# Kernel optimization log

Hardware: AMD Instinct MI355X
Metric: run time of the kernel (lower is better)

Reference implementation:

```python
import jax, jax.numpy as jnp
from jax import lax
import numpy as np

B, T, C_IN, H, W = 2, 4, 128, 64, 64
D_MODEL, N_Q, N_POINTS, PATCH, N_LAYERS = 256, 300, 8, 3, 6


def _sine_pos(Hh, Ww, d, temperature=10000.0):
    # mask is all-False, so cumsum of ones -> arange(1..H)/H * 2pi
    two_pi = 2.0 * np.pi
    yn = (jnp.arange(1, Hh + 1, dtype=jnp.float32) / (Hh + 1e-6)) * two_pi
    xn = (jnp.arange(1, Ww + 1, dtype=jnp.float32) / (Ww + 1e-6)) * two_pi
    q = d // 4
    i = jnp.arange(q, dtype=jnp.float32)
    dim_t = temperature ** (2.0 * jnp.floor(i / 2.0) / q)
    py = yn[:, None] / dim_t
    px = xn[:, None] / dim_t
    py = jnp.stack([jnp.sin(py), jnp.cos(py)], axis=-1).reshape(Hh, 2 * q)
    px = jnp.stack([jnp.sin(px), jnp.cos(px)], axis=-1).reshape(Ww, 2 * q)
    pos = jnp.concatenate([
        jnp.broadcast_to(py[:, None, :], (Hh, Ww, 2 * q)),
        jnp.broadcast_to(px[None, :, :], (Hh, Ww, 2 * q)),
    ], axis=-1)
    return jnp.transpose(pos, (2, 0, 1))  # [d,H,W]


def _sample_scale(fmap, ref, ps):
    # fmap [B,C,h,w]; ref [B,nQ,nP,2] in [0,1]. Bilinear grid_sample,
    # padding_mode='border', align_corners=True -> direct gather (no replication).
    Bc, C, h, w = fmap.shape
    half = (ps - 1) / 2.0
    off = jnp.linspace(-half, half, ps, dtype=jnp.float32)
    oy, ox = jnp.meshgrid(off, off, indexing='ij')  # [ps,ps]
    gx = ref[..., 0, None, None] * 2.0 - 1.0 + ox * (2.0 / w)  # [B,nQ,nP,ps,ps]
    gy = ref[..., 1, None, None] * 2.0 - 1.0 + oy * (2.0 / h)
    x = jnp.clip((gx + 1.0) * 0.5 * (w - 1), 0.0, w - 1.0)
    y = jnp.clip((gy + 1.0) * 0.5 * (h - 1), 0.0, h - 1.0)
    x0 = jnp.floor(x); y0 = jnp.floor(y)
    wx = x - x0; wy = y - y0
    x0i = x0.astype(jnp.int32); y0i = y0.astype(jnp.int32)
    x1i = jnp.minimum(x0i + 1, w - 1); y1i = jnp.minimum(y0i + 1, h - 1)

    def per_b(fb, y0b, x0b, y1b, x1b, wxb, wyb):
        v00 = fb[:, y0b, x0b]  # [C,nQ,nP,ps,ps]
        v01 = fb[:, y0b, x1b]
        v10 = fb[:, y1b, x0b]
        v11 = fb[:, y1b, x1b]
        return (v00 * (1 - wxb) * (1 - wyb) + v01 * wxb * (1 - wyb)
                + v10 * (1 - wxb) * wyb + v11 * wxb * wyb)

    out = jax.vmap(per_b)(fmap, y0i, x0i, y1i, x1i, wx, wy)  # [B,C,nQ,nP,ps,ps]
    return jnp.transpose(out, (0, 2, 3, 4, 5, 1))  # [B,nQ,nP,ps,ps,C]


def reference(feat, pred_boxes_init, w_tf, b_tf, w_in, b_in, w_lat, b_lat, w_sm, b_sm,
              q_embed, q_pos, Wq, bq, Wo, bo, Wp1, bp1, Wp2, bp2,
              w_r1, b_r1, w_r2, b_r2, w_b1, b_b1, w_b2, b_b2, w_cls, b_cls):
    Bb, Tt, Cin, Hh, Ww = feat.shape
    d = w_in.shape[0]
    nP = w_r2.shape[0] // 2
    ps = int(round((Wp1.shape[-1] // d) ** 0.5))
    # temporal fuse: Conv3d kernel (3,1,1), padding (1,0,0)
    x = lax.conv_general_dilated(jnp.transpose(feat, (0, 2, 1, 3, 4)), w_tf,
                                 (1, 1, 1), [(1, 1), (0, 0), (0, 0)],
                                 dimension_numbers=('NCDHW', 'OIDHW', 'NCDHW'))
    x = x + b_tf[None, :, None, None, None]
    x = x.mean(axis=2)  # [B,Cin,H,W]
    x = jnp.einsum('bchw,dc->bdhw', x, w_in) + b_in[None, :, None, None]
    x = x + _sine_pos(Hh, Ww, d)[None]
    # FPN over scales {1,2,4}: avg_pool -> 1x1 lateral -> 3x3 smooth
    feats = []
    for i, s in enumerate((1, 2, 4)):
        xi = x if s == 1 else x.reshape(Bb, d, Hh // s, s, Ww // s, s).mean(axis=(3, 5))
        xi = jnp.einsum('bchw,oc->bohw', xi, w_lat[i]) + b_lat[i][None, :, None, None]
        xi = lax.conv_general_dilated(xi, w_sm[i], (1, 1), [(1, 1), (1, 1)],
                                      dimension_numbers=('NCHW', 'OIHW', 'NCHW'))
        xi = xi + b_sm[i][None, :, None, None]
        feats.append(xi)
    nQ = q_embed.shape[0]
    queries = jnp.broadcast_to((q_embed + q_pos)[None], (Bb, nQ, d))
    boxes = pred_boxes_init
    inv_sqrt_d = 1.0 / float(np.sqrt(d))
    for l in range(Wq.shape[0]):
        h1 = jax.nn.relu(jnp.einsum('bqd,od->bqo', queries, w_r1) + b_r1)
        ro = jnp.tanh(jnp.einsum('bqd,od->bqo', h1, w_r2) + b_r2)
        ro = ro.reshape(Bb, nQ, nP, 2) * 0.5
        ref = jnp.clip(boxes[:, :, None, :2] + ro, 0.0, 1.0)
        sampled = jnp.concatenate([_sample_scale(f, ref, ps) for f in feats], axis=2)
        sampled = sampled[:, :, :nP]  # truncate multi-scale concat back to nP
        flat = sampled.reshape(Bb, nQ, nP, ps * ps * d)
        pv = jax.nn.relu(jnp.einsum('bqpi,oi->bqpo', flat, Wp1[l]) + bp1[l])
        pv = jnp.einsum('bqpd,od->bqpo', pv, Wp2[l]) + bp2[l]
        kv = pv.mean(axis=2)  # [B,nP_q,d] -> [B,nQ,d]
        q = jnp.einsum('bqd,od->bqo', queries, Wq[l]) + bq[l]
        attn = jax.nn.softmax(jnp.einsum('bqd,bkd->bqk', q, kv) * inv_sqrt_d, axis=-1)
        out = jnp.einsum('bqk,bkd->bqd', attn, kv)
        queries = queries + (jnp.einsum('bqd,od->bqo', out, Wo[l]) + bo[l])
        hb = jax.nn.relu(jnp.einsum('bqd,od->bqo', queries, w_b1) + b_b1)
        delta = jax.nn.sigmoid(jnp.einsum('bqd,od->bqo', hb, w_b2) + b_b2)
        boxes = jnp.clip(boxes + 0.1 * jnp.tanh(delta - 0.5), 0.0, 1.0)
    logits = (jnp.einsum('bqd,od->bqo', queries, w_cls) + b_cls)[..., 0]
    return logits, boxes


def setup_inputs() -> dict:
    key = jax.random.key(0)
    keys = iter(jax.random.split(key, 48))

    def nrm(shape, s=0.02):
        return jax.random.normal(next(keys), shape, dtype=jnp.float32) * s

    inp = {
        'feat': jax.random.normal(next(keys), (B, T, C_IN, H, W), dtype=jnp.float32),
        'pred_boxes_init': jax.random.uniform(next(keys), (B, N_Q, 4), dtype=jnp.float32),
        'w_tf': nrm((C_IN, C_IN, 3, 1, 1)), 'b_tf': jnp.zeros((C_IN,), jnp.float32),
        'w_in': nrm((D_MODEL, C_IN)), 'b_in': jnp.zeros((D_MODEL,), jnp.float32),
        'w_lat': nrm((3, D_MODEL, D_MODEL)), 'b_lat': jnp.zeros((3, D_MODEL), jnp.float32),
        'w_sm': nrm((3, D_MODEL, D_MODEL, 3, 3)), 'b_sm': jnp.zeros((3, D_MODEL), jnp.float32),
        'q_embed': nrm((N_Q, D_MODEL), 1.0), 'q_pos': nrm((N_Q, D_MODEL), 1.0),
        'Wq': nrm((N_LAYERS, D_MODEL, D_MODEL)), 'bq': jnp.zeros((N_LAYERS, D_MODEL), jnp.float32),
        'Wo': nrm((N_LAYERS, D_MODEL, D_MODEL)), 'bo': jnp.zeros((N_LAYERS, D_MODEL), jnp.float32),
        'Wp1': nrm((N_LAYERS, D_MODEL, PATCH * PATCH * D_MODEL)), 'bp1': jnp.zeros((N_LAYERS, D_MODEL), jnp.float32),
        'Wp2': nrm((N_LAYERS, D_MODEL, D_MODEL)), 'bp2': jnp.zeros((N_LAYERS, D_MODEL), jnp.float32),
        'w_r1': nrm((D_MODEL, D_MODEL)), 'b_r1': jnp.zeros((D_MODEL,), jnp.float32),
        'w_r2': nrm((2 * N_POINTS, D_MODEL)), 'b_r2': jnp.zeros((2 * N_POINTS,), jnp.float32),
        'w_b1': nrm((D_MODEL, D_MODEL)), 'b_b1': jnp.zeros((D_MODEL,), jnp.float32),
        'w_b2': nrm((4, D_MODEL)), 'b_b2': jnp.zeros((4,), jnp.float32),
        'w_cls': nrm((1, D_MODEL)), 'b_cls': jnp.zeros((1,), jnp.float32),
    }
    return inp
```

## Files before the change

### kernel.cpp

```cpp
#include <hip/hip_runtime.h>
#include <hip/hip_bf16.h>
#include <math.h>

#define BB 2
#define TT 4
#define CIN 128
#define DM 256
#define NQ 300
#define NP 8
#define PS 3
#define NL 6
#define HW 4096
#define KP 2304

typedef __attribute__((ext_vector_type(8))) short short8;
typedef __attribute__((ext_vector_type(4))) short short4_t;
typedef __attribute__((ext_vector_type(4))) float f32x4;
typedef unsigned short ushort_t;

static __device__ __forceinline__ ushort_t f2bf(float f) {
  __hip_bfloat16 h = __float2bfloat16(f);
  return *reinterpret_cast<ushort_t*>(&h);
}
static __device__ __forceinline__ float bf2f(ushort_t u) {
  return __uint_as_float(((unsigned)u) << 16);
}

__global__ void k_prep(const float* __restrict__ w_in, const float* __restrict__ w_lat,
                       const float* __restrict__ w_b1,
                       const float* __restrict__ w_r1, const float* __restrict__ Wp1,
                       ushort_t* __restrict__ win_bf, ushort_t* __restrict__ wlat_bf,
                       ushort_t* __restrict__ wb1_bf,
                       ushort_t* __restrict__ wr1_bf, ushort_t* __restrict__ wp1_bf,
                       const float* __restrict__ w_tf, ushort_t* __restrict__ tct,
                       const float* __restrict__ w_sm, ushort_t* __restrict__ wsm_bf,
                       const float* __restrict__ Wp2, const float* __restrict__ Wo,
                       const float* __restrict__ bq, const float* __restrict__ bp2,
                       const float* __restrict__ bo,
                       float* __restrict__ bqt, float* __restrict__ bfuse,
                       uint4* __restrict__ x2p_zero,
                       const float* __restrict__ b_tf, const float* __restrict__ b_in,
                       float* __restrict__ bias_comb,
                       const float* __restrict__ qe, const float* __restrict__ qp,
                       const float* __restrict__ pb, float* __restrict__ queries,
                       ushort_t* __restrict__ qbf, float* __restrict__ boxes,
                       const float* __restrict__ feat, ushort_t* __restrict__ featT) {
  __shared__ float ldsF[64][65];
  float* bt = &ldsF[0][0];
  int b = blockIdx.x, t = threadIdx.x;
  if (b < 3680) {
    int i = b * 256 + t;
    const float* s; ushort_t* d; int base;
    if (i < 8192)         { s = w_in;  d = win_bf;  base = 0; }
    else if (i < 24576)   { s = w_lat; d = wlat_bf; base = 8192; }
    else if (i < 40960)   { s = w_b1;  d = wb1_bf;  base = 24576; }
    else if (i < 57344)   { s = w_r1;  d = wr1_bf;  base = 40960; }
    else                  { s = Wp1;   d = wp1_bf;  base = 57344; }
    int j = i - base;
    float4 v = ((const float4*)s)[j];
    short4_t o;
    o[0] = (short)f2bf(v.x); o[1] = (short)f2bf(v.y);
    o[2] = (short)f2bf(v.z); o[3] = (short)f2bf(v.w);
    *(short4_t*)(d + j * 4) = o;
  } else if (b < 3936) {
    int i = (b - 3680) * 256 + t;
    int k = i >> 7, c = i & 127;
    int u = k >> 7, ci = k & 127;
    const float* wp = w_tf + ((size_t)(c * 128 + ci)) * 3;
    float w0 = wp[0], w1 = wp[1], w2 = wp[2];
    float coef = (u == 0) ? (w0 + w1) : (u == 3) ? (w1 + w2) : (w0 + w1 + w2);
    tct[(size_t)k * 128 + c] = f2bf(0.25f * coef);
  } else if (b < 6240) {
    int i = (b - 3936) * 256 + t;
    int n = i / KP;
    int r = i - n * KP;
    int tp = r >> 8, c = r & 255;
    wsm_bf[i] = f2bf(w_sm[((size_t)(n * 256 + c)) * 9 + tp]);
  } else if (b < 6252) {
    int i = (b - 6240) * 256 + t;
    if (i < 1536) {
      int l = i >> 8, d = i & 255;
      float a = 0.f;
      for (int o = 0; o < 256; ++o)
        a += bq[l * 256 + o] * Wp2[((size_t)(l * 256 + o)) * 256 + d];
      bqt[i] = a;
    } else {
      int j = i - 1536;
      int l = j >> 8, o2 = j & 255;
      float a = bo[l * 256 + o2];
      for (int o = 0; o < 256; ++o)
        a += bp2[l * 256 + o] * Wo[((size_t)(l * 256 + o2)) * 256 + o];
      bfuse[j] = a;
    }
  } else if (b < 7341) {
    int j = (b - 6252) * 256 + t;
    if (j < 278784) x2p_zero[j] = make_uint4(0u, 0u, 0u, 0u);
  } else if (b < 7342) {
    int d = t;
    if (d < 128) bt[d] = b_tf[d];
    __syncthreads();
    float a = b_in[d];
    for (int c = 0; c < 128; ++c) a += w_in[d * 128 + c] * bt[c];
    bias_comb[d] = a;
  } else if (b < 7942) {
    int i = (b - 7342) * 256 + t;
    if (i < BB * NQ * DM) {
      int rd = i % (NQ * DM);
      float v = qe[rd] + qp[rd];
      queries[i] = v;
      qbf[i] = f2bf(v);
    }
    if (i < BB * NQ * 4) boxes[i] = pb[i];
  } else {
    int idx = b - 7942;
    int gs = idx & 127;
    int k0 = (idx >> 7) * 64;
    int bb = gs >> 6;
    int s0 = (gs & 63) * 64;
    int kk = t >> 2, sc0 = (t & 3) * 16;
    {
      int k = k0 + kk;
      int u = k >> 7, ci = k & 127;
      const float* src = feat + (((size_t)(bb * 4 + u) * 128 + ci) << 12) + s0 + sc0;
#pragma unroll
      for (int j = 0; j < 4; ++j) {
        float4 v = *(const float4*)(src + j * 4);
        ldsF[kk][sc0 + j * 4 + 0] = v.x;
        ldsF[kk][sc0 + j * 4 + 1] = v.y;
        ldsF[kk][sc0 + j * 4 + 2] = v.z;
        ldsF[kk][sc0 + j * 4 + 3] = v.w;
      }
    }
    __syncthreads();
#pragma unroll
    for (int p = 0; p < 2; ++p) {
      int idx2 = p * 256 + t;
      int s_l = idx2 >> 3, kc = (idx2 & 7) * 8;
      short8 v;
#pragma unroll
      for (int j = 0; j < 8; ++j) v[j] = (short)f2bf(ldsF[kc + j][s_l]);
      *(short8*)(featT + (size_t)(bb * 4096 + s0 + s_l) * 512 + k0 + kc) = v;
    }
  }
}

__global__ __launch_bounds__(256) void k_wcompose(const float* __restrict__ Wp2,
                                                  const float* __restrict__ Wq,
                                                  const float* __restrict__ Wo,
                                                  ushort_t* __restrict__ wqt,
                                                  ushort_t* __restrict__ wfuseT) {
  __shared__ ushort_t As[64 * 36];
  __shared__ ushort_t Bs[64 * 36];
  int z = blockIdx.z, l = z % 6;
  const float* Asrc = Wp2 + (size_t)l * 65536;
  const float* Bsrc = ((z < 6) ? Wq : Wo) + (size_t)l * 65536;
  ushort_t* C = ((z < 6) ? wqt : wfuseT) + (size_t)l * 65536;
  bool btr = (z < 6);
  int tid = threadIdx.x;
  int bm = blockIdx.x * 64, bn = blockIdx.y * 64;
  int w = tid >> 6, lane = tid & 63;
  int wm = (w & 1) * 32, wn = (w >> 1) * 32;
  int q = lane >> 4, ml = lane & 15;
  f32x4 acc[2][2] = {};
  int oo = tid >> 3, mg = (tid & 7) * 8;
  int nr = tid >> 2, kg = (tid & 3) * 8;
  for (int k0 = 0; k0 < 256; k0 += 32) {
    {
      const float* sp = Asrc + (size_t)(k0 + oo) * 256 + bm + mg;
      float4 f0 = *(const float4*)sp;
      float4 f1 = *(const float4*)(sp + 4);
      ushort_t* dst = As + oo;
      dst[(mg + 0) * 36] = f2bf(f0.x); dst[(mg + 1) * 36] = f2bf(f0.y);
      dst[(mg + 2) * 36] = f2bf(f0.z); dst[(mg + 3) * 36] = f2bf(f0.w);
      dst[(mg + 4) * 36] = f2bf(f1.x); dst[(mg + 5) * 36] = f2bf(f1.y);
      dst[(mg + 6) * 36] = f2bf(f1.z); dst[(mg + 7) * 36] = f2bf(f1.w);
    }
    if (btr) {
      const float* sp = Bsrc + (size_t)(k0 + oo) * 256 + bn + mg;
      float4 f0 = *(const float4*)sp;
      float4 f1 = *(const float4*)(sp + 4);
      ushort_t* dst = Bs + oo;
      dst[(mg + 0) * 36] = f2bf(f0.x); dst[(mg + 1) * 36] = f2bf(f0.y);
      dst[(mg + 2) * 36] = f2bf(f0.z); dst[(mg + 3) * 36] = f2bf(f0.w);
      dst[(mg + 4) * 36] = f2bf(f1.x); dst[(mg + 5) * 36] = f2bf(f1.y);
      dst[(mg + 6) * 36] = f2bf(f1.z); dst[(mg + 7) * 36] = f2bf(f1.w);
    } else {
      const float* sp = Bsrc + (size_t)(bn + nr) * 256 + k0 + kg;
      float4 f0 = *(const float4*)sp;
      float4 f1 = *(const float4*)(sp + 4);
      short8 v;
      v[0] = (short)f2bf(f0.x); v[1] = (short)f2bf(f0.y);
      v[2] = (short)f2bf(f0.z); v[3] = (short)f2bf(f0.w);
      v[4] = (short)f2bf(f1.x); v[5] = (short)f2bf(f1.y);
      v[6] = (short)f2bf(f1.z); v[7] = (short)f2bf(f1.w);
      *(short8*)(Bs + nr * 36 + kg) = v;
    }
    __syncthreads();
    short8 a0 = *(const short8*)(As + (wm + ml) * 36 + q * 8);
    short8 a1 = *(const short8*)(As + (wm + 16 + ml) * 36 + q * 8);
    short8 b0 = *(const short8*)(Bs + (wn + ml) * 36 + q * 8);
    short8 b1 = *(const short8*)(Bs + (wn + 16 + ml) * 36 + q * 8);
    acc[0][0] = __builtin_amdgcn_mfma_f32_16x16x32_bf16(a0, b0, acc[0][0], 0, 0, 0);
    acc[0][1] = __builtin_amdgcn_mfma_f32_16x16x32_bf16(a0, b1, acc[0][1], 0, 0, 0);
    acc[1][0] = __builtin_amdgcn_mfma_f32_16x16x32_bf16(a1, b0, acc[1][0], 0, 0, 0);
    acc[1][1] = __builtin_amdgcn_mfma_f32_16x16x32_bf16(a1, b1, acc[1][1], 0, 0, 0);
    __syncthreads();
  }
#pragma unroll
  for (int i = 0; i < 2; ++i)
#pragma unroll
    for (int j = 0; j < 2; ++j) {
      int cn = bn + wn + j * 16 + ml;
#pragma unroll
      for (int r = 0; r < 4; ++r) {
        int rm = bm + wm + i * 16 + q * 4 + r;
        C[(size_t)rm * 256 + cn] = f2bf(acc[i][j][r]);
      }
    }
}

__global__ __launch_bounds__(256) void k_feat2(const ushort_t* __restrict__ featT,
                                               const ushort_t* __restrict__ wcomb,
                                               const float* __restrict__ biasc,
                                               ushort_t* __restrict__ xcl) {
  __shared__ ushort_t As[32 * 72];
  __shared__ ushort_t Bs[64 * 72];
  __shared__ float dimt_s[256];
  int tid = threadIdx.x;
  {
    int dd = tid & 127;
    int ii = dd >> 1;
    dimt_s[tid] = powf(10000.0f, (2.0f * (float)(ii >> 1)) / 64.0f);
  }
  int bm = blockIdx.x * 32, bn = blockIdx.y * 64;
  int w = tid >> 6, lane = tid & 63;
  int wm = (w & 1) * 16, wn = (w >> 1) * 32;
  int q = lane >> 4, ml = lane & 15;
  int sra = tid >> 3, sca = (tid & 7) * 8;
  int srb = tid >> 2, scb = (tid & 3) * 16;
  const ushort_t* Ag = featT + (size_t)(bm + sra) * 512 + sca;
  const ushort_t* Wg = wcomb + (size_t)(bn + srb) * 512 + scb;
  f32x4 acc[2] = {};
  short8 av = *(const short8*)Ag;
  short8 wv0 = *(const short8*)Wg;
  short8 wv1 = *(const short8*)(Wg + 8);
  for (int k0 = 0; k0 < 512; k0 += 64) {
    *(short8*)(As + sra * 72 + sca) = av;
    *(short8*)(Bs + srb * 72 + scb) = wv0;
    *(short8*)(Bs + srb * 72 + scb + 8) = wv1;
    __syncthreads();
    if (k0 + 64 < 512) {
      av = *(const short8*)(Ag + k0 + 64);
      wv0 = *(const short8*)(Wg + k0 + 64);
      wv1 = *(const short8*)(Wg + k0 + 72);
    }
#pragma unroll
    for (int h = 0; h < 2; ++h) {
      int kc = h * 32 + q * 8;
      short8 a = *(const short8*)(As + (wm + ml) * 72 + kc);
      short8 b0 = *(const short8*)(Bs + (wn + ml) * 72 + kc);
      short8 b1 = *(const short8*)(Bs + (wn + 16 + ml) * 72 + kc);
      acc[0] = __builtin_amdgcn_mfma_f32_16x16x32_bf16(a, b0, acc[0], 0, 0, 0);
      acc[1] = __builtin_amdgcn_mfma_f32_16x16x32_bf16(a, b1, acc[1], 0, 0, 0);
    }
    __syncthreads();
  }
  const float FKT = 6.28318530717958647692f / 64.000001f;
#pragma unroll
  for (int j = 0; j < 2; ++j) {
    int cn = bn + wn + j * 16 + ml;
    float dimt = dimt_s[cn];
    float bC = biasc[cn];
    bool isx = cn >= 128;
    bool isc = cn & 1;
#pragma unroll
    for (int r = 0; r < 4; ++r) {
      int rm = bm + wm + q * 4 + r;
      int s = rm & 4095;
      int y = s >> 6, x = s & 63;
      float ang = (float)((isx ? x : y) + 1) * FKT / dimt;
      float pos = isc ? cosf(ang) : sinf(ang);
      xcl[(size_t)rm * 256 + cn] = f2bf(acc[j][r] + bC + pos);
    }
  }
}

template <int ACT, int OUTMODE, int MG>
__global__ __launch_bounds__(256) void k_gemm_bf16(const ushort_t* __restrict__ A,
                                                   const ushort_t* __restrict__ W,
                                                   const float* __restrict__ bias,
                                                   const float* __restrict__ res,
                                                   float* __restrict__ Cf,
                                                   ushort_t* __restrict__ Cb,
                                                   int M, int N, int K) {
  __shared__ ushort_t As[64 * 72];
  __shared__ ushort_t Bs[64 * 72];
  int tid = threadIdx.x;
  int bm = blockIdx.x * 64, bn = blockIdx.y * 64;
  int w = tid >> 6, lane = tid & 63;
  int wm = (w & 1) * 32, wn = (w >> 1) * 32;
  int q = lane >> 4, ml = lane & 15;
  f32x4 acc[2][2] = {};
  int srow = tid >> 2, scol = (tid & 3) * 16;
  int ga = bm + srow;
  if (MG) ga = min(ga, M - 1);
  const ushort_t* Ag = A + (size_t)ga * K + scol;
  const ushort_t* Wg = W + (size_t)(bn + srow) * K + scol;
  short8 av0 = *(const short8*)(Ag);
  short8 av1 = *(const short8*)(Ag + 8);
  short8 wv0 = *(const short8*)(Wg);
  short8 wv1 = *(const short8*)(Wg + 8);
  for (int k0 = 0; k0 < K; k0 += 64) {
    *(short8*)(As + srow * 72 + scol) = av0;
    *(short8*)(As + srow * 72 + scol + 8) = av1;
    *(short8*)(Bs + srow * 72 + scol) = wv0;
    *(short8*)(Bs + srow * 72 + scol + 8) = wv1;
    __syncthreads();
    if (k0 + 64 < K) {
      av0 = *(const short8*)(Ag + k0 + 64);
      av1 = *(const short8*)(Ag + k0 + 72);
      wv0 = *(const short8*)(Wg + k0 + 64);
      wv1 = *(const short8*)(Wg + k0 + 72);
    }
#pragma unroll
    for (int h = 0; h < 2; ++h) {
      int kc = h * 32 + q * 8;
      short8 a0 = *(const short8*)(As + (wm + ml) * 72 + kc);
      short8 a1 = *(const short8*)(As + (wm + 16 + ml) * 72 + kc);
      short8 b0 = *(const short8*)(Bs + (wn + ml) * 72 + kc);
      short8 b1 = *(const short8*)(Bs + (wn + 16 + ml) * 72 + kc);
      acc[0][0] = __builtin_amdgcn_mfma_f32_16x16x32_bf16(a0, b0, acc[0][0], 0, 0, 0);
      acc[0][1] = __builtin_amdgcn_mfma_f32_16x16x32_bf16(a0, b1, acc[0][1], 0, 0, 0);
      acc[1][0] = __builtin_amdgcn_mfma_f32_16x16x32_bf16(a1, b0, acc[1][0], 0, 0, 0);
      acc[1][1] = __builtin_amdgcn_mfma_f32_16x16x32_bf16(a1, b1, acc[1][1], 0, 0, 0);
    }
    __syncthreads();
  }
#pragma unroll
  for (int i = 0; i < 2; ++i) {
#pragma unroll
    for (int j = 0; j < 2; ++j) {
      int cn = bn + wn + j * 16 + ml;
      float bsv = bias ? bias[cn] : 0.f;
#pragma unroll
      for (int r = 0; r < 4; ++r) {
        int rm = bm + wm + i * 16 + q * 4 + r;
        if (MG && rm >= M) continue;
        float v = acc[i][j][r] + bsv;
        if (OUTMODE == 0) {
          if (ACT == 1) v = fmaxf(v, 0.f);
          Cf[(size_t)rm * N + cn] = v;
        } else if (OUTMODE == 1) {
          int b = rm >> 12, rem = rm & 4095;
          int y = rem >> 6, xx = rem & 63;
          Cb[(((size_t)(b * 66 + y + 1)) * 66 + xx + 1) * 256 + cn] = f2bf(v);
        } else if (OUTMODE == 6) {
          Cb[(size_t)rm * N + cn] = f2bf(v);
        }
      }
    }
  }
}

template <int OUTMODE>
__global__ __launch_bounds__(256) void k_gemm32(const ushort_t* __restrict__ A,
                                                const ushort_t* __restrict__ W,
                                                const float* __restrict__ bias,
                                                const float* __restrict__ res,
                                                float* __restrict__ Cf,
                                                ushort_t* __restrict__ Cb,
                                                int M, int K,
                                                const ushort_t* __restrict__ W2,
                                                const float* __restrict__ bias2,
                                                const ushort_t* __restrict__ W3,
                                                const float* __restrict__ bias3) {
  __shared__ ushort_t As[32 * 72];
  __shared__ ushort_t Bs[64 * 72];
  int tid = threadIdx.x;
  int bm = blockIdx.x * 32, bn = blockIdx.y * 64;
  int w = tid >> 6, lane = tid & 63;
  int wm = (w & 1) * 16, wn = (w >> 1) * 32;
  int q = lane >> 4, ml = lane & 15;
  int sra = tid >> 3, sca = (tid & 7) * 8;
  int srb = tid >> 2, scb = (tid & 3) * 16;
  int ga = min(bm + sra, M - 1);
  const ushort_t* Ag = A + (size_t)ga * K + sca;
  const ushort_t* Wg;
  if (OUTMODE == 7) {
    int seg = bn >> 8;
    const ushort_t* Wb = (seg == 0) ? W : ((seg == 1) ? W2 : W3);
    Wg = Wb + (size_t)((bn & 255) + srb) * K + scb;
  } else {
    const ushort_t* Wb = (bn < 256) ? W : W2;
    Wg = Wb + (size_t)((bn & 255) + srb) * K + scb;
  }
  f32x4 acc[2] = {};
  short8 av = *(const short8*)(Ag);
  short8 wv0 = *(const short8*)(Wg);
  short8 wv1 = *(const short8*)(Wg + 8);
  for (int k0 = 0; k0 < K; k0 += 64) {
    *(short8*)(As + sra * 72 + sca) = av;
    *(short8*)(Bs + srb * 72 + scb) = wv0;
    *(short8*)(Bs + srb * 72 + scb + 8) = wv1;
    __syncthreads();
    if (k0 + 64 < K) {
      av = *(const short8*)(Ag + k0 + 64);
      wv0 = *(const short8*)(Wg + k0 + 64);
      wv1 = *(const short8*)(Wg + k0 + 72);
    }
#pragma unroll
    for (int h = 0; h < 2; ++h) {
      int kc = h * 32 + q * 8;
      short8 a = *(const short8*)(As + (wm + ml) * 72 + kc);
      short8 b0 = *(const short8*)(Bs + (wn + ml) * 72 + kc);
      short8 b1 = *(const short8*)(Bs + (wn + 16 + ml) * 72 + kc);
      acc[0] = __builtin_amdgcn_mfma_f32_16x16x32_bf16(a, b0, acc[0], 0, 0, 0);
      acc[1] = __builtin_amdgcn_mfma_f32_16x16x32_bf16(a, b1, acc[1], 0, 0, 0);
    }
    __syncthreads();
  }
#pragma unroll
  for (int j = 0; j < 2; ++j) {
    int cn = bn + wn + j * 16 + ml;
    float bsv;
    if (OUTMODE == 7) {
      int seg = cn >> 8;
      bsv = ((seg == 0) ? bias : ((seg == 1) ? bias2 : bias3))[cn & 255];
    } else {
      bsv = ((cn < 256) ? bias : bias2)[cn & 255];
    }
#pragma unroll
    for (int r = 0; r < 4; ++r) {
      int rm = bm + wm + q * 4 + r;
      if (rm >= M) continue;
      float v = acc[j][r] + bsv;
      if (OUTMODE == 4) {
        if (cn < 256) Cf[(size_t)rm * 256 + cn] = fmaxf(v, 0.f);
        else Cb[(size_t)rm * 256 + (cn & 255)] = f2bf(v);
      } else {
        if (cn < 256) Cf[(size_t)rm * 256 + cn] = fmaxf(v, 0.f);
        else if (cn < 512) ((float*)Cb)[(size_t)rm * 256 + (cn & 255)] = fmaxf(v, 0.f);
        else ((ushort_t*)res)[(size_t)rm * 256 + (cn & 255)] = f2bf(v);
      }
    }
  }
}

__global__ __launch_bounds__(256) void k_wp1_split(const ushort_t* __restrict__ A,
                                                   const ushort_t* __restrict__ W,
                                                   ushort_t* __restrict__ part) {
  __shared__ ushort_t As[64 * 72];
  __shared__ ushort_t Bs[64 * 72];
  int tid = threadIdx.x;
  int bm = blockIdx.x * 64, bn = blockIdx.y * 64;
  int kz = blockIdx.z * 768;
  int w = tid >> 6, lane = tid & 63;
  int wm = (w & 1) * 32, wn = (w >> 1) * 32;
  int q = lane >> 4, ml = lane & 15;
  int srow = tid >> 2, scol = (tid & 3) * 16;
  const ushort_t* Ag = A + (size_t)(bm + srow) * KP + kz + scol;
  const ushort_t* Wg = W + (size_t)(bn + srow) * KP + kz + scol;
  f32x4 acc[2][2] = {};
  short8 av0 = *(const short8*)(Ag);
  short8 av1 = *(const short8*)(Ag + 8);
  short8 wv0 = *(const short8*)(Wg);
  short8 wv1 = *(const short8*)(Wg + 8);
  for (int k0 = 0; k0 < 768; k0 += 64) {
    *(short8*)(As + srow * 72 + scol) = av0;
    *(short8*)(As + srow * 72 + scol + 8) = av1;
    *(short8*)(Bs + srow * 72 + scol) = wv0;
    *(short8*)(Bs + srow * 72 + scol + 8) = wv1;
    __syncthreads();
    if (k0 + 64 < 768) {
      av0 = *(const short8*)(Ag + k0 + 64);
      av1 = *(const short8*)(Ag + k0 + 72);
      wv0 = *(const short8*)(Wg + k0 + 64);
      wv1 = *(const short8*)(Wg + k0 + 72);
    }
#pragma unroll
    for (int h = 0; h < 2; ++h) {
      int kc = h * 32 + q * 8;
      short8 a0 = *(const short8*)(As + (wm + ml) * 72 + kc);
      short8 a1 = *(const short8*)(As + (wm + 16 + ml) * 72 + kc);
      short8 b0 = *(const short8*)(Bs + (wn + ml) * 72 + kc);
      short8 b1 = *(const short8*)(Bs + (wn + 16 + ml) * 72 + kc);
      acc[0][0] = __builtin_amdgcn_mfma_f32_16x16x32_bf16(a0, b0, acc[0][0], 0, 0, 0);
      acc[0][1] = __builtin_amdgcn_mfma_f32_16x16x32_bf16(a0, b1, acc[0][1], 0, 0, 0);
      acc[1][0] = __builtin_amdgcn_mfma_f32_16x16x32_bf16(a1, b0, acc[1][0], 0, 0, 0);
      acc[1][1] = __builtin_amdgcn_mfma_f32_16x16x32_bf16(a1, b1, acc[1][1], 0, 0, 0);
    }
    __syncthreads();
  }
  ushort_t* pz = part + (size_t)blockIdx.z * 4800 * 256;
#pragma unroll
  for (int i = 0; i < 2; ++i)
#pragma unroll
    for (int j = 0; j < 2; ++j) {
      int cn = bn + wn + j * 16 + ml;
#pragma unroll
      for (int r = 0; r < 4; ++r) {
        int rm = bm + wm + i * 16 + q * 4 + r;
        pz[(size_t)rm * 256 + cn] = f2bf(acc[i][j][r]);
      }
    }
}

__global__ __launch_bounds__(256) void k_wp1_reduce(const ushort_t* __restrict__ part,
                                                    const float* __restrict__ bias,
                                                    ushort_t* __restrict__ pvm) {
  int row = blockIdx.x;
  int d = threadIdx.x;
  float b = bias[d];
  float s = 0.f;
#pragma unroll
  for (int p = 0; p < 8; ++p) {
    size_t idx = (size_t)(row * 8 + p) * 256 + d;
    float v = bf2f(part[idx]) + bf2f(part[idx + (size_t)4800 * 256]) +
              bf2f(part[idx + (size_t)2 * 4800 * 256]) + b;
    s += fmaxf(v, 0.f);
  }
  pvm[(size_t)row * 256 + d] = f2bf(s * 0.125f);
}

__global__ __launch_bounds__(256) void k_conv3(const ushort_t* __restrict__ x2p,
                                               const ushort_t* __restrict__ wsm,
                                               const float* __restrict__ bsm,
                                               ushort_t* __restrict__ fcl) {
  __shared__ ushort_t As[32 * 72];
  __shared__ ushort_t Bs[64 * 72];
  int tid = threadIdx.x;
  int bm = blockIdx.x * 32, bn = blockIdx.y * 64;
  int w = tid >> 6, lane = tid & 63;
  int wm = (w & 1) * 16, wn = (w >> 1) * 32;
  int q = lane >> 4, ml = lane & 15;
  int sra = tid >> 3, sca = (tid & 7) * 8;
  int srb = tid >> 2, scb = (tid & 3) * 16;
  int sA = bm + sra;
  int b = sA >> 12, rem = sA & 4095;
  size_t pbase = ((size_t)(b * 66 + (rem >> 6)) * 66 + (rem & 63)) * 256;
  const ushort_t* Wg = wsm + (size_t)(bn + srb) * KP + scb;
  auto loadA = [&](int k0) {
    int ka = k0 + sca;
    int t9 = ka >> 8;
    int ky = t9 / 3, kx = t9 - ky * 3;
    return *(const short8*)(x2p + pbase + (size_t)(ky * 66 + kx) * 256 + (ka & 255));
  };
  f32x4 acc[2] = {};
  short8 av = loadA(0);
  short8 wv0 = *(const short8*)(Wg);
  short8 wv1 = *(const short8*)(Wg + 8);
  for (int k0 = 0; k0 < KP; k0 += 64) {
    *(short8*)(As + sra * 72 + sca) = av;
    *(short8*)(Bs + srb * 72 + scb) = wv0;
    *(short8*)(Bs + srb * 72 + scb + 8) = wv1;
    __syncthreads();
    if (k0 + 64 < KP) {
      av = loadA(k0 + 64);
      wv0 = *(const short8*)(Wg + k0 + 64);
      wv1 = *(const short8*)(Wg + k0 + 72);
    }
#pragma unroll
    for (int h = 0; h < 2; ++h) {
      int kc = h * 32 + q * 8;
      short8 a = *(const short8*)(As + (wm + ml) * 72 + kc);
      short8 b0 = *(const short8*)(Bs + (wn + ml) * 72 + kc);
      short8 b1 = *(const short8*)(Bs + (wn + 16 + ml) * 72 + kc);
      acc[0] = __builtin_amdgcn_mfma_f32_16x16x32_bf16(a, b0, acc[0], 0, 0, 0);
      acc[1] = __builtin_amdgcn_mfma_f32_16x16x32_bf16(a, b1, acc[1], 0, 0, 0);
    }
    __syncthreads();
  }
#pragma unroll
  for (int j = 0; j < 2; ++j) {
    int cn = bn + wn + j * 16 + ml;
    float bsv = bsm[cn];
#pragma unroll
    for (int r = 0; r < 4; ++r) {
      int rm = bm + wm + q * 4 + r;
      fcl[(size_t)rm * 256 + cn] = f2bf(acc[j][r] + bsv);
    }
  }
}

__global__ __launch_bounds__(256) void k_sample(const ushort_t* __restrict__ fcl,
                                                const float* __restrict__ h1,
                                                const float* __restrict__ w_r2,
                                                const float* __restrict__ b_r2,
                                                const float* __restrict__ boxesIn,
                                                float* __restrict__ boxesOut,
                                                const float* __restrict__ hb,
                                                const float* __restrict__ w_b2,
                                                const float* __restrict__ b_b2,
                                                ushort_t* __restrict__ flat) {
  __shared__ float pr[8];
  __shared__ float bc2[2];
  __shared__ float nb2[2];
  int blk = blockIdx.x;
  int row = blk >> 3, p = blk & 7;
  int b = row / NQ;
  int tid = threadIdx.x;
  int w = tid >> 6, lane = tid & 63;
  if (hb) {
    float4 hv = *(const float4*)(hb + (size_t)row * 256 + lane * 4);
    float4 wv = *(const float4*)(w_b2 + (size_t)w * 256 + lane * 4);
    float aa = hv.x * wv.x + hv.y * wv.y + hv.z * wv.z + hv.w * wv.w;
#pragma unroll
    for (int s = 32; s > 0; s >>= 1) aa += __shfl_down(aa, s, 64);
    if (lane == 0) {
      aa += b_b2[w];
      float delta = 1.0f / (1.0f + expf(-aa));
      float v = boxesIn[row * 4 + w] + 0.1f * tanhf(delta - 0.5f);
      v = fminf(fmaxf(v, 0.f), 1.f);
      if (w < 2) nb2[w] = v;
      if (p == 0) boxesOut[row * 4 + w] = v;
    }
  } else if (tid < 2) {
    nb2[tid] = boxesIn[row * 4 + tid];
  }
  float h = h1[(size_t)row * 256 + tid];
  float px = h * w_r2[(size_t)(2 * p) * 256 + tid];
  float py = h * w_r2[(size_t)(2 * p + 1) * 256 + tid];
#pragma unroll
  for (int s = 32; s > 0; s >>= 1) {
    px += __shfl_down(px, s, 64);
    py += __shfl_down(py, s, 64);
  }
  if (lane == 0) { pr[w * 2] = px; pr[w * 2 + 1] = py; }
  __syncthreads();
  if (tid == 0) {
    float sx = pr[0] + pr[2] + pr[4] + pr[6] + b_r2[2 * p];
    float sy = pr[1] + pr[3] + pr[5] + pr[7] + b_r2[2 * p + 1];
    float rx = nb2[0] + 0.5f * tanhf(sx);
    float ry = nb2[1] + 0.5f * tanhf(sy);
    bc2[0] = fminf(fmaxf(rx, 0.f), 1.f);
    bc2[1] = fminf(fmaxf(ry, 0.f), 1.f);
  }
  __syncthreads();
  float rx = bc2[0], ry = bc2[1];
  const ushort_t* fb = fcl + (size_t)b * HW * DM;
  ushort_t* op = flat + (size_t)blk * KP;
  int c4 = (tid & 63) * 4;
  int g = tid >> 6;
  int p0 = (g == 0) ? 0 : (1 + 2 * g);
  int p1 = (g == 0) ? 3 : (3 + 2 * g);
  for (int p9 = p0; p9 < p1; ++p9) {
    int jy = (p9 >= 6) ? 2 : ((p9 >= 3) ? 1 : 0);
    int jx = p9 - jy * 3;
    float yy = (ry + (float)(jy - 1) * (1.0f / 64.0f)) * 63.0f;
    yy = fminf(fmaxf(yy, 0.f), 63.0f);
    float y0f = floorf(yy);
    float wy = yy - y0f;
    int y0 = (int)y0f;
    int y1 = min(y0 + 1, 63);
    float xx = (rx + (float)(jx - 1) * (1.0f / 64.0f)) * 63.0f;
    xx = fminf(fmaxf(xx, 0.f), 63.0f);
    float x0f = floorf(xx);
    float wx = xx - x0f;
    int x0 = (int)x0f;
    int x1 = min(x0 + 1, 63);
    short4_t v00 = *(const short4_t*)(fb + (y0 * 64 + x0) * DM + c4);
    short4_t v01 = *(const short4_t*)(fb + (y0 * 64 + x1) * DM + c4);
    short4_t v10 = *(const short4_t*)(fb + (y1 * 64 + x0) * DM + c4);
    short4_t v11 = *(const short4_t*)(fb + (y1 * 64 + x1) * DM + c4);
    short4_t ov;
#pragma unroll
    for (int jj = 0; jj < 4; ++jj) {
      float v = bf2f((ushort_t)v00[jj]) * (1.f - wx) * (1.f - wy) +
                bf2f((ushort_t)v01[jj]) * wx * (1.f - wy) +
                bf2f((ushort_t)v10[jj]) * (1.f - wx) * wy +
                bf2f((ushort_t)v11[jj]) * wx * wy;
      ov[jj] = (short)f2bf(v);
    }
    *(short4_t*)(op + p9 * DM + c4) = ov;
  }
}

__global__ __launch_bounds__(256) void k_attn(const ushort_t* __restrict__ qt,
                                              const ushort_t* __restrict__ pvm,
                                              const ushort_t* __restrict__ wfT,
                                              const float* __restrict__ bfuse_l,
                                              float* __restrict__ queries,
                                              ushort_t* __restrict__ qbf) {
  __shared__ float qs[256];
  __shared__ float sc[512];
  __shared__ float red[256];
  __shared__ float pr4[1024];
  int row = blockIdx.x;
  int b = row / NQ;
  int tid = threadIdx.x;
  qs[tid] = bf2f(qt[(size_t)row * DM + tid]);
  __syncthreads();
  const ushort_t* kvB = pvm + (size_t)b * NQ * DM;
#pragma unroll
  for (int s2 = 0; s2 < 2; ++s2) {
    int k = tid + s2 * 256;
    float v = -1e30f;
    if (k < NQ) {
      const ushort_t* kp = kvB + (size_t)k * DM;
      float a = 0.f;
#pragma unroll
      for (int d = 0; d < 256; d += 8) {
        short8 k8 = *(const short8*)(kp + d);
        const float* qd = qs + d;
        a += bf2f((ushort_t)k8[0]) * qd[0];
        a += bf2f((ushort_t)k8[1]) * qd[1];
        a += bf2f((ushort_t)k8[2]) * qd[2];
        a += bf2f((ushort_t)k8[3]) * qd[3];
        a += bf2f((ushort_t)k8[4]) * qd[4];
        a += bf2f((ushort_t)k8[5]) * qd[5];
        a += bf2f((ushort_t)k8[6]) * qd[6];
        a += bf2f((ushort_t)k8[7]) * qd[7];
      }
      v = a * (1.0f / 16.0f);
    }
    sc[k] = v;
  }
  __syncthreads();
  red[tid] = fmaxf(sc[tid], sc[tid + 256]);
  __syncthreads();
  for (int st = 128; st > 0; st >>= 1) {
    if (tid < st) red[tid] = fmaxf(red[tid], red[tid + st]);
    __syncthreads();
  }
  float mx = red[0];
  __syncthreads();
  float e0 = (tid < NQ) ? expf(sc[tid] - mx) : 0.f;
  float e1 = (tid + 256 < NQ) ? expf(sc[tid + 256] - mx) : 0.f;
  sc[tid] = e0;
  sc[tid + 256] = e1;
  red[tid] = e0 + e1;
  __syncthreads();
  for (int st = 128; st > 0; st >>= 1) {
    if (tid < st) red[tid] += red[tid + st];
    __syncthreads();
  }
  float inv = 1.0f / red[0];
  __syncthreads();
  float acc = 0.f;
#pragma unroll 4
  for (int k = 0; k < NQ; ++k)
    acc += sc[k] * bf2f(kvB[(size_t)k * DM + tid]);
  qs[tid] = acc * inv;
  __syncthreads();
  int oq = (tid & 63) * 4, dq = (tid >> 6) * 64;
  float a0 = 0.f, a1 = 0.f, a2 = 0.f, a3 = 0.f;
  const ushort_t* wp = wfT + (size_t)dq * 256 + oq;
#pragma unroll 8
  for (int dd = 0; dd < 64; ++dd) {
    float cc = qs[dq + dd];
    short4_t wv = *(const short4_t*)(wp + (size_t)dd * 256);
    a0 += cc * bf2f((ushort_t)wv[0]);
    a1 += cc * bf2f((ushort_t)wv[1]);
    a2 += cc * bf2f((ushort_t)wv[2]);
    a3 += cc * bf2f((ushort_t)wv[3]);
  }
  float* pb4 = pr4 + (tid >> 6) * 256 + oq;
  pb4[0] = a0; pb4[1] = a1; pb4[2] = a2; pb4[3] = a3;
  __syncthreads();
  float v = pr4[tid] + pr4[256 + tid] + pr4[512 + tid] + pr4[768 + tid] +
            bfuse_l[tid] + queries[(size_t)row * DM + tid];
  queries[(size_t)row * DM + tid] = v;
  qbf[(size_t)row * DM + tid] = f2bf(v);
}

__global__ __launch_bounds__(256) void k_boxf(const float* __restrict__ hb,
                                              const float* __restrict__ w_b2,
                                              const float* __restrict__ b_b2,
                                              float* __restrict__ boxes,
                                              int last,
                                              const float* __restrict__ queries,
                                              const float* __restrict__ w_cls,
                                              const float* __restrict__ b_cls,
                                              float* __restrict__ out) {
  __shared__ float nb[4];
  int row = blockIdx.x;
  int tid = threadIdx.x;
  int j = tid >> 6, lane = tid & 63;
  float4 hv = *(const float4*)(hb + (size_t)row * 256 + lane * 4);
  float4 wv = *(const float4*)(w_b2 + (size_t)j * 256 + lane * 4);
  float aa = hv.x * wv.x + hv.y * wv.y + hv.z * wv.z + hv.w * wv.w;
#pragma unroll
  for (int s = 32; s > 0; s >>= 1) aa += __shfl_down(aa, s, 64);
  if (lane == 0) {
    aa += b_b2[j];
    float delta = 1.0f / (1.0f + expf(-aa));
    float v = boxes[row * 4 + j] + 0.1f * tanhf(delta - 0.5f);
    v = fminf(fmaxf(v, 0.f), 1.f);
    boxes[row * 4 + j] = v;
    nb[j] = v;
  }
  if (last) {
    __syncthreads();
    if (j == 0) {
      float4 qv = *(const float4*)(queries + (size_t)row * 256 + lane * 4);
      float4 cv = *(const float4*)(w_cls + lane * 4);
      float a2 = qv.x * cv.x + qv.y * cv.y + qv.z * cv.z + qv.w * cv.w;
#pragma unroll
      for (int s = 32; s > 0; s >>= 1) a2 += __shfl_down(a2, s, 64);
      if (lane == 0) out[row] = a2 + b_cls[0];
    } else if (j == 1 && lane < 4) {
      out[600 + row * 4 + lane] = nb[lane];
    }
  }
}

extern "C" void kernel_launch(void* const* d_in, const int* in_sizes, int n_in,
                              void* d_out, int out_size, void* d_ws, size_t ws_size,
                              hipStream_t stream) {
  const float* feat   = (const float*)d_in[0];
  const float* pb     = (const float*)d_in[1];
  const float* w_tf   = (const float*)d_in[2];
  const float* b_tf   = (const float*)d_in[3];
  const float* w_in   = (const float*)d_in[4];
  const float* b_in   = (const float*)d_in[5];
  const float* w_lat  = (const float*)d_in[6];
  const float* b_lat  = (const float*)d_in[7];
  const float* w_sm   = (const float*)d_in[8];
  const float* b_sm   = (const float*)d_in[9];
  const float* q_embed= (const float*)d_in[10];
  const float* q_pos  = (const float*)d_in[11];
  const float* Wq     = (const float*)d_in[12];
  const float* bq     = (const float*)d_in[13];
  const float* Wo     = (const float*)d_in[14];
  const float* bo     = (const float*)d_in[15];
  const float* Wp1    = (const float*)d_in[16];
  const float* bp1    = (const float*)d_in[17];
  const float* Wp2    = (const float*)d_in[18];
  const float* bp2    = (const float*)d_in[19];
  const float* w_r1   = (const float*)d_in[20];
  const float* b_r1   = (const float*)d_in[21];
  const float* w_r2   = (const float*)d_in[22];
  const float* b_r2   = (const float*)d_in[23];
  const float* w_b1   = (const float*)d_in[24];
  const float* b_b1   = (const float*)d_in[25];
  const float* w_b2   = (const float*)d_in[26];
  const float* b_b2   = (const float*)d_in[27];
  const float* w_cls  = (const float*)d_in[28];
  const float* b_cls  = (const float*)d_in[29];
  float* out = (float*)d_out;

  float* ws = (float*)d_ws;
  size_t off = 0;
  auto alloc = [&](size_t n) { float* p = ws + off; off += n; return p; };
  ushort_t* flat    = (ushort_t*)alloc(5529600);
  ushort_t* part    = (ushort_t*)alloc(1843200);
  ushort_t* featT   = (ushort_t*)alloc(2097152);
  ushort_t* xcl     = (ushort_t*)alloc(1048576);
  ushort_t* x2p     = (ushort_t*)alloc(1115136);
  ushort_t* fcl     = (ushort_t*)alloc(1048576);
  ushort_t* wcomb   = (ushort_t*)alloc(65536);
  ushort_t* tct     = (ushort_t*)alloc(32768);
  ushort_t* win_bf  = (ushort_t*)alloc(16384);
  float*    biasc   = alloc(256);
  ushort_t* wlat_bf = (ushort_t*)alloc(32768);
  ushort_t* wsm_bf  = (ushort_t*)alloc(294912);
  ushort_t* wp1_bf  = (ushort_t*)alloc(1769472);
  ushort_t* wb1_bf  = (ushort_t*)alloc(32768);
  ushort_t* wr1_bf  = (ushort_t*)alloc(32768);
  ushort_t* wqt_bf  = (ushort_t*)alloc(196608);
  ushort_t* wfuseT  = (ushort_t*)alloc(196608);
  float*    bqt     = alloc(1536);
  float*    bfuse   = alloc(1536);
  float* queries = alloc(153600);
  ushort_t* qbf  = (ushort_t*)alloc(76800);
  float* h1      = alloc(153600);
  ushort_t* qt   = (ushort_t*)alloc(76800);
  float* hb      = alloc(153600);
  ushort_t* pvm  = (ushort_t*)alloc(76800);
  float* boxesA  = alloc(2400);
  float* boxesB  = alloc(2400);
  (void)ws_size; (void)in_sizes; (void)n_in; (void)out_size;

  k_prep<<<8966, 256, 0, stream>>>(w_in, w_lat, w_b1, w_r1, Wp1,
                                   win_bf, wlat_bf, wb1_bf, wr1_bf, wp1_bf,
                                   w_tf, tct, w_sm, wsm_bf,
                                   Wp2, Wo, bq, bp2, bo, bqt, bfuse,
                                   (uint4*)x2p, b_tf, b_in, biasc,
                                   q_embed, q_pos, pb, queries, qbf, boxesA,
                                   feat, featT);
  k_gemm_bf16<0, 6, 0><<<dim3(4, 8), 256, 0, stream>>>(win_bf, tct, nullptr, nullptr,
                                                       nullptr, wcomb, 256, 512, 128);
  k_wcompose<<<dim3(4, 4, 12), 256, 0, stream>>>(Wp2, Wq, Wo, wqt_bf, wfuseT);

  k_feat2<<<dim3(256, 4), 256, 0, stream>>>(featT, wcomb, biasc, xcl);
  k_gemm_bf16<0, 1, 0><<<dim3(128, 4), 256, 0, stream>>>(xcl, wlat_bf, b_lat, nullptr,
                                                         nullptr, x2p, BB * HW, 256, 256);
  k_conv3<<<dim3(256, 4), 256, 0, stream>>>(x2p, wsm_bf, b_sm, fcl);

  const int M6 = BB * NQ;
  const int Mp = BB * NQ * NP;
  dim3 g600w((M6 + 31) / 32, 8);
  dim3 g600m((M6 + 31) / 32, 12);
  dim3 gsk(Mp / 64, 4, 3);

  k_gemm32<4><<<g600w, 256, 0, stream>>>(qbf, wr1_bf, b_r1, nullptr, h1,
                                         qt, M6, 256,
                                         wqt_bf, bqt, nullptr, nullptr);
  float* bcur = boxesA;
  float* bnext = boxesB;
  for (int l = 0; l < NL; ++l) {
    const float* hbp = (l == 0) ? nullptr : hb;
    k_sample<<<Mp, 256, 0, stream>>>(fcl, h1, w_r2, b_r2, bcur, bnext,
                                     hbp, w_b2, b_b2, flat);
    if (l > 0) { float* tmp = bcur; bcur = bnext; bnext = tmp; }
    k_wp1_split<<<gsk, 256, 0, stream>>>(flat, wp1_bf + (size_t)l * 256 * KP, part);
    k_wp1_reduce<<<600, 256, 0, stream>>>(part, bp1 + (size_t)l * DM, pvm);
    k_attn<<<M6, 256, 0, stream>>>(qt, pvm, wfuseT + (size_t)l * 65536,
                                   bfuse + l * 256, queries, qbf);
    int ln = (l + 1) % NL;
    k_gemm32<7><<<g600m, 256, 0, stream>>>(qbf, wb1_bf, b_b1, (const float*)qt,
                                           hb, (ushort_t*)h1, M6, 256,
                                           wr1_bf, b_r1,
                                           wqt_bf + (size_t)ln * 65536,
                                           bqt + ln * 256);
  }
  k_boxf<<<M6, 256, 0, stream>>>(hb, w_b2, b_b2, bcur, 1,
                                 queries, w_cls, b_cls, out);
}
```

Before: 664.2 us.

## Widen Wp1 split GEMM tile to 64x128 and coalesce w_sm transpose via LDS

The split-K Wp1 GEMM now uses 512-thread blocks that each compute a 64x128 output tile, halving the grid in N. Each A tile is loaded once and reused across twice as many output columns, so A traffic drops. Separately, the w_sm bf16 transpose in the prep kernel stages one output channel's 2304 weights in LDS with coalesced float4 loads instead of doing strided per-element gathers, which cuts the prep grid size. The tradeoffs are fewer blocks in the GEMM grid and more LDS per block.

```diff
diff --git a/kernel.cpp b/kernel.cpp
--- a/kernel.cpp
+++ b/kernel.cpp
@@ -70,14 +70,22 @@
     float w0 = wp[0], w1 = wp[1], w2 = wp[2];
     float coef = (u == 0) ? (w0 + w1) : (u == 3) ? (w1 + w2) : (w0 + w1 + w2);
     tct[(size_t)k * 128 + c] = f2bf(0.25f * coef);
-  } else if (b < 6240) {
-    int i = (b - 3936) * 256 + t;
-    int n = i / KP;
-    int r = i - n * KP;
-    int tp = r >> 8, c = r & 255;
-    wsm_bf[i] = f2bf(w_sm[((size_t)(n * 256 + c)) * 9 + tp]);
-  } else if (b < 6252) {
-    int i = (b - 6240) * 256 + t;
+  } else if (b < 4192) {
+    int n = b - 3936;
+    float* l2 = &ldsF[0][0];
+    const float* src = w_sm + (size_t)n * KP;
+    for (int idx = t; idx < 576; idx += 256) {
+      float4 v = ((const float4*)src)[idx];
+      l2[idx * 4 + 0] = v.x; l2[idx * 4 + 1] = v.y;
+      l2[idx * 4 + 2] = v.z; l2[idx * 4 + 3] = v.w;
+    }
+    __syncthreads();
+    ushort_t* dst = wsm_bf + (size_t)n * KP;
+#pragma unroll
+    for (int tp = 0; tp < 9; ++tp)
+      dst[tp * 256 + t] = f2bf(l2[t * 9 + tp]);
+  } else if (b < 4204) {
+    int i = (b - 4192) * 256 + t;
     if (i < 1536) {
       int l = i >> 8, d = i & 255;
       float a = 0.f;
@@ -92,18 +100,18 @@
         a += bp2[l * 256 + o] * Wo[((size_t)(l * 256 + o2)) * 256 + o];
       bfuse[j] = a;
     }
-  } else if (b < 7341) {
-    int j = (b - 6252) * 256 + t;
+  } else if (b < 5293) {
+    int j = (b - 4204) * 256 + t;
     if (j < 278784) x2p_zero[j] = make_uint4(0u, 0u, 0u, 0u);
-  } else if (b < 7342) {
+  } else if (b < 5294) {
     int d = t;
     if (d < 128) bt[d] = b_tf[d];
     __syncthreads();
     float a = b_in[d];
     for (int c = 0; c < 128; ++c) a += w_in[d * 128 + c] * bt[c];
     bias_comb[d] = a;
-  } else if (b < 7942) {
-    int i = (b - 7342) * 256 + t;
+  } else if (b < 5894) {
+    int i = (b - 5294) * 256 + t;
     if (i < BB * NQ * DM) {
       int rd = i % (NQ * DM);
       float v = qe[rd] + qp[rd];
@@ -112,7 +120,7 @@
     }
     if (i < BB * NQ * 4) boxes[i] = pb[i];
   } else {
-    int idx = b - 7942;
+    int idx = b - 5894;
     int gs = idx & 127;
     int k0 = (idx >> 7) * 64;
     int bb = gs >> 6;
@@ -446,34 +454,32 @@
   }
 }
 
-__global__ __launch_bounds__(256) void k_wp1_split(const ushort_t* __restrict__ A,
+__global__ __launch_bounds__(512) void k_wp1_split(const ushort_t* __restrict__ A,
                                                    const ushort_t* __restrict__ W,
                                                    ushort_t* __restrict__ part) {
   __shared__ ushort_t As[64 * 72];
-  __shared__ ushort_t Bs[64 * 72];
+  __shared__ ushort_t Bs[128 * 72];
   int tid = threadIdx.x;
-  int bm = blockIdx.x * 64, bn = blockIdx.y * 64;
+  int bm = blockIdx.x * 64, bn = blockIdx.y * 128;
   int kz = blockIdx.z * 768;
   int w = tid >> 6, lane = tid & 63;
   int wm = (w & 1) * 32, wn = (w >> 1) * 32;
   int q = lane >> 4, ml = lane & 15;
-  int srow = tid >> 2, scol = (tid & 3) * 16;
-  const ushort_t* Ag = A + (size_t)(bm + srow) * KP + kz + scol;
-  const ushort_t* Wg = W + (size_t)(bn + srow) * KP + kz + scol;
+  int srA = tid >> 3, scA = (tid & 7) * 8;
+  int srB = tid >> 2, scB = (tid & 3) * 16;
+  const ushort_t* Ag = A + (size_t)(bm + srA) * KP + kz + scA;
+  const ushort_t* Wg = W + (size_t)(bn + srB) * KP + kz + scB;
   f32x4 acc[2][2] = {};
-  short8 av0 = *(const short8*)(Ag);
-  short8 av1 = *(const short8*)(Ag + 8);
+  short8 av = *(const short8*)(Ag);
   short8 wv0 = *(const short8*)(Wg);
   short8 wv1 = *(const short8*)(Wg + 8);
   for (int k0 = 0; k0 < 768; k0 += 64) {
-    *(short8*)(As + srow * 72 + scol) = av0;
-    *(short8*)(As + srow * 72 + scol + 8) = av1;
-    *(short8*)(Bs + srow * 72 + scol) = wv0;
-    *(short8*)(Bs + srow * 72 + scol + 8) = wv1;
+    *(short8*)(As + srA * 72 + scA) = av;
+    *(short8*)(Bs + srB * 72 + scB) = wv0;
+    *(short8*)(Bs + srB * 72 + scB + 8) = wv1;
     __syncthreads();
     if (k0 + 64 < 768) {
-      av0 = *(const short8*)(Ag + k0 + 64);
-      av1 = *(const short8*)(Ag + k0 + 72);
+      av = *(const short8*)(Ag + k0 + 64);
       wv0 = *(const short8*)(Wg + k0 + 64);
       wv1 = *(const short8*)(Wg + k0 + 72);
     }
@@ -871,7 +877,7 @@
   float* boxesB  = alloc(2400);
   (void)ws_size; (void)in_sizes; (void)n_in; (void)out_size;
 
-  k_prep<<<8966, 256, 0, stream>>>(w_in, w_lat, w_b1, w_r1, Wp1,
+  k_prep<<<6918, 256, 0, stream>>>(w_in, w_lat, w_b1, w_r1, Wp1,
                                    win_bf, wlat_bf, wb1_bf, wr1_bf, wp1_bf,
                                    w_tf, tct, w_sm, wsm_bf,
                                    Wp2, Wo, bq, bp2, bo, bqt, bfuse,
@@ -891,7 +897,7 @@
   const int Mp = BB * NQ * NP;
   dim3 g600w((M6 + 31) / 32, 8);
   dim3 g600m((M6 + 31) / 32, 12);
-  dim3 gsk(Mp / 64, 4, 3);
+  dim3 gsk(Mp / 64, 2, 3);
 
   k_gemm32<4><<<g600w, 256, 0, stream>>>(qbf, wr1_bf, b_r1, nullptr, h1,
                                          qt, M6, 256,
@@ -903,7 +909,7 @@
     k_sample<<<Mp, 256, 0, stream>>>(fcl, h1, w_r2, b_r2, bcur, bnext,
                                      hbp, w_b2, b_b2, flat);
     if (l > 0) { float* tmp = bcur; bcur = bnext; bnext = tmp; }
-    k_wp1_split<<<gsk, 256, 0, stream>>>(flat, wp1_bf + (size_t)l * 256 * KP, part);
+    k_wp1_split<<<gsk, 512, 0, stream>>>(flat, wp1_bf + (size_t)l * 256 * KP, part);
     k_wp1_reduce<<<600, 256, 0, stream>>>(part, bp1 + (size_t)l * DM, pvm);
     k_attn<<<M6, 256, 0, stream>>>(qt, pvm, wfuseT + (size_t)l * 65536,
                                    bfuse + l * 256, queries, qbf);
```

Result: faster. 647.0 us (-2.6%).
